# Kernel optimization log

Measured on AMD Instinct MI355X. Metric: run time of the kernel, lower is better.

Reference implementation:

```python
import jax, jax.numpy as jnp
import numpy as np

TIME_MASK_MAX_LEN = 35
TIME_MASK_STEP = 100
FREQ_MASK_MAX_LEN = 30
P = 0.5
LOG_EPS = np.float32(np.log(np.finfo(np.float64).eps))  # log(torch.finfo(float).eps)


def setup_inputs() -> dict:
    key = jax.random.key(0)
    x = jax.random.normal(key, (16, 25600, 256), dtype=jnp.float32)
    return {"x": x}


def _build_mask(key, C, T, F):
    """Boolean mask [C, T, F]; True where x is overwritten with log(eps)."""
    Cm = C - 3                      # last 3 channels are never masked
    nb = T // TIME_MASK_STEP        # number of time blocks per channel
    k1, k2, k3, k4 = jax.random.split(key, 4)
    # per (channel, block) random cutoffs, matching torch.randint semantics
    tlen = jax.random.randint(k1, (Cm, nb), 0, TIME_MASK_MAX_LEN)              # [0, 35)
    tstart = jnp.floor(jax.random.uniform(k2, (Cm, nb)) *
                       (TIME_MASK_STEP - tlen)).astype(jnp.int32)              # [0, step-len)
    flen = jax.random.randint(k3, (Cm, nb), 0, FREQ_MASK_MAX_LEN)              # [0, 30)
    fstart = jnp.floor(jax.random.uniform(k4, (Cm, nb)) *
                       (F - flen)).astype(jnp.int32)                           # [0, F-len)

    t = jnp.arange(T)
    block = t // TIME_MASK_STEP
    local = t - block * TIME_MASK_STEP                       # position within block
    valid = block < nb                                       # frames past last full block untouched
    bidx = jnp.minimum(block, nb - 1)

    ts = tstart[:, bidx]                                     # [Cm, T]
    tl = tlen[:, bidx]
    time_in = (local[None, :] >= ts) & (local[None, :] < ts + tl) & valid[None, :]

    fs = fstart[:, bidx]                                     # [Cm, T]
    fl = flen[:, bidx]
    f = jnp.arange(F)
    mask = time_in[:, :, None] & (f[None, None, :] >= fs[:, :, None]) & \
           (f[None, None, :] < (fs + fl)[:, :, None])        # [Cm, T, F]
    # last 3 channels unmasked
    return jnp.concatenate([mask, jnp.zeros((3, T, F), dtype=bool)], axis=0)


def reference(x):
    C, T, F = x.shape
    key = jax.random.key(42)
    kcoin, kmask = jax.random.split(key)
    apply_mask = jax.random.uniform(kcoin, ()) <= P          # np.random.rand() > p -> skip
    mask = _build_mask(kmask, C, T, F) & apply_mask
    return jnp.where(mask, LOG_EPS, x)
```

## Files before the change

### kernel.cpp

```cpp
#include <hip/hip_runtime.h>
#include <cstdint>
#include <cstddef>
#include <math.h>


#define C_TOT 16
#define C_MASKED 13
#define T_TOT 25600
#define F_TOT 256
#define NB 256
#define TSTEP 100

static constexpr float LOG_EPS = -36.04365338911715f;

typedef float f32x4 __attribute__((ext_vector_type(4)));

struct U2 { unsigned a, b; };

__host__ __device__ constexpr unsigned rotl_(unsigned x, int d) {
  return (x << d) | (x >> (32 - d));
}

__host__ __device__ constexpr U2 tf(unsigned k0, unsigned k1, unsigned x0, unsigned x1) {
  const unsigned ks2 = k0 ^ k1 ^ 0x1BD11BDAu;
  x0 += k0; x1 += k1;
  x0 += x1; x1 = rotl_(x1,13) ^ x0;
  x0 += x1; x1 = rotl_(x1,15) ^ x0;
  x0 += x1; x1 = rotl_(x1,26) ^ x0;
  x0 += x1; x1 = rotl_(x1, 6) ^ x0;
  x0 += k1; x1 += ks2 + 1u;
  x0 += x1; x1 = rotl_(x1,17) ^ x0;
  x0 += x1; x1 = rotl_(x1,29) ^ x0;
  x0 += x1; x1 = rotl_(x1,16) ^ x0;
  x0 += x1; x1 = rotl_(x1,24) ^ x0;
  x0 += ks2; x1 += k0 + 2u;
  x0 += x1; x1 = rotl_(x1,13) ^ x0;
  x0 += x1; x1 = rotl_(x1,15) ^ x0;
  x0 += x1; x1 = rotl_(x1,26) ^ x0;
  x0 += x1; x1 = rotl_(x1, 6) ^ x0;
  x0 += k0; x1 += k1 + 3u;
  x0 += x1; x1 = rotl_(x1,17) ^ x0;
  x0 += x1; x1 = rotl_(x1,29) ^ x0;
  x0 += x1; x1 = rotl_(x1,16) ^ x0;
  x0 += x1; x1 = rotl_(x1,24) ^ x0;
  x0 += k1; x1 += ks2 + 4u;
  x0 += x1; x1 = rotl_(x1,13) ^ x0;
  x0 += x1; x1 = rotl_(x1,15) ^ x0;
  x0 += x1; x1 = rotl_(x1,26) ^ x0;
  x0 += x1; x1 = rotl_(x1, 6) ^ x0;
  x0 += ks2; x1 += k0 + 5u;
  return U2{x0, x1};
}

constexpr U2 KCOIN = tf(0u, 42u, 0u, 0u);
constexpr U2 KMASK = tf(0u, 42u, 0u, 1u);
constexpr U2 K1 = tf(KMASK.a, KMASK.b, 0u, 0u);
constexpr U2 K2 = tf(KMASK.a, KMASK.b, 0u, 1u);
constexpr U2 K3 = tf(KMASK.a, KMASK.b, 0u, 2u);
constexpr U2 K4 = tf(KMASK.a, KMASK.b, 0u, 3u);
constexpr U2 CE = tf(KCOIN.a, KCOIN.b, 0u, 0u);
constexpr unsigned COIN_BITS = CE.a ^ CE.b;
constexpr bool APPLY = (COIN_BITS >> 9) <= 4194304u;

__device__ __forceinline__ float u01(unsigned bits) {
  return __uint_as_float((bits >> 9) | 0x3f800000u) - 1.0f;
}

__device__ __forceinline__ void mask_params(int j, int& ts, int& te, int& fs, int& fe) {
  const unsigned uj = (unsigned)j;
  unsigned h, l, bits;
  U2 e;
  e = tf(K1.a, K1.b, 0u, uj);          h = e.a ^ e.b;
  e = tf(K1.a, K1.b, 0u, uj + 3328u);  l = e.a ^ e.b;
  const unsigned tl = ((h % 35u) * 11u + (l % 35u)) % 35u;
  e = tf(K2.a, K2.b, 0u, uj);          bits = e.a ^ e.b;
  const int tstart = (int)floorf(u01(bits) * (float)(TSTEP - (int)tl));
  e = tf(K3.a, K3.b, 0u, uj);          h = e.a ^ e.b;
  e = tf(K3.a, K3.b, 0u, uj + 3328u);  l = e.a ^ e.b;
  const unsigned fl = ((h % 30u) * 16u + (l % 30u)) % 30u;
  e = tf(K4.a, K4.b, 0u, uj);          bits = e.a ^ e.b;
  const int fstart = (int)floorf(u01(bits) * (float)(F_TOT - (int)fl));
  ts = tstart; te = tstart + (int)tl;
  fs = fstart; fe = fstart + (int)fl;
}

__global__ void __launch_bounds__(256)
speca_kernel(const float* __restrict__ x, float* __restrict__ y) {
  const int bid = blockIdx.x;
  const int c = bid >> 8;
  const int b = bid & 255;
  const size_t base = ((size_t)c * T_TOT + (size_t)b * TSTEP) * F_TOT;
  const f32x4* __restrict__ in4 = (const f32x4*)(x + base);
  f32x4* __restrict__ o4 = (f32x4*)(y + base);

  int ts = 0, te = -1, fs = 0, fe = -1;
  if (APPLY && c < C_MASKED) {
    mask_params((c << 8) | b, ts, te, fs, fe);
  }

  const int tid = (int)threadIdx.x;
#pragma unroll 5
  for (int k = 0; k < (TSTEP * F_TOT) / 4 / 256; ++k) {
    const int i = k * 256 + tid;
    f32x4 v = __builtin_nontemporal_load(&in4[i]);
    const int r = i >> 6;
    if (r >= ts && r < te) {
      const int f0 = (i & 63) << 2;
      if (f0     >= fs && f0     < fe) v[0] = LOG_EPS;
      if (f0 + 1 >= fs && f0 + 1 < fe) v[1] = LOG_EPS;
      if (f0 + 2 >= fs && f0 + 2 < fe) v[2] = LOG_EPS;
      if (f0 + 3 >= fs && f0 + 3 < fe) v[3] = LOG_EPS;
    }
    __builtin_nontemporal_store(v, &o4[i]);
  }
}

extern "C" void kernel_launch(void* const* d_in, const int* in_sizes, int n_in,
                              void* d_out, int out_size, void* d_ws, size_t ws_size,
                              hipStream_t stream) {
  const float* x = (const float*)d_in[0];
  float* y = (float*)d_out;
  hipLaunchKernelGGL(speca_kernel, dim3(C_TOT * NB), dim3(256), 0, stream, x, y);
}
```

Before: 155.1 us.

## Replace fused mask kernel with device memcpy plus sparse patch kernel

The full streaming read-modify-write kernel is replaced by a hipMemcpyAsync device-to-device copy of the whole tensor, followed by a small kernel that writes LOG_EPS only into the masked rectangles. Each patch block recomputes its mask parameters and stores at most about 35x30 floats. This hands the bulk traffic to the runtime copy path (possibly a DMA engine or a tuned blit kernel) and drops the per-element mask checks, at the cost of a second launch and a dependency on how fast the copy path is.

```diff
diff --git a/kernel.cpp b/kernel.cpp
--- a/kernel.cpp
+++ b/kernel.cpp
@@ -12,8 +12,6 @@
 #define TSTEP 100
 
 static constexpr float LOG_EPS = -36.04365338911715f;
-
-typedef float f32x4 __attribute__((ext_vector_type(4)));
 
 struct U2 { unsigned a, b; };
 
@@ -84,34 +82,18 @@
   fs = fstart; fe = fstart + (int)fl;
 }
 
-__global__ void __launch_bounds__(256)
-speca_kernel(const float* __restrict__ x, float* __restrict__ y) {
+__global__ void __launch_bounds__(64)
+patch_kernel(float* __restrict__ y) {
   const int bid = blockIdx.x;
   const int c = bid >> 8;
   const int b = bid & 255;
-  const size_t base = ((size_t)c * T_TOT + (size_t)b * TSTEP) * F_TOT;
-  const f32x4* __restrict__ in4 = (const f32x4*)(x + base);
-  f32x4* __restrict__ o4 = (f32x4*)(y + base);
-
-  int ts = 0, te = -1, fs = 0, fe = -1;
-  if (APPLY && c < C_MASKED) {
-    mask_params((c << 8) | b, ts, te, fs, fe);
-  }
-
-  const int tid = (int)threadIdx.x;
-#pragma unroll 5
-  for (int k = 0; k < (TSTEP * F_TOT) / 4 / 256; ++k) {
-    const int i = k * 256 + tid;
-    f32x4 v = __builtin_nontemporal_load(&in4[i]);
-    const int r = i >> 6;
-    if (r >= ts && r < te) {
-      const int f0 = (i & 63) << 2;
-      if (f0     >= fs && f0     < fe) v[0] = LOG_EPS;
-      if (f0 + 1 >= fs && f0 + 1 < fe) v[1] = LOG_EPS;
-      if (f0 + 2 >= fs && f0 + 2 < fe) v[2] = LOG_EPS;
-      if (f0 + 3 >= fs && f0 + 3 < fe) v[3] = LOG_EPS;
-    }
-    __builtin_nontemporal_store(v, &o4[i]);
+  int ts, te, fs, fe;
+  mask_params(bid, ts, te, fs, fe);
+  const int f = fs + (int)threadIdx.x;
+  if (f >= fe) return;
+  float* __restrict__ chunk = y + ((size_t)c * T_TOT + (size_t)b * TSTEP) * F_TOT;
+  for (int r = ts; r < te; ++r) {
+    chunk[(size_t)r * F_TOT + f] = LOG_EPS;
   }
 }
 
@@ -120,5 +102,9 @@
                               hipStream_t stream) {
   const float* x = (const float*)d_in[0];
   float* y = (float*)d_out;
-  hipLaunchKernelGGL(speca_kernel, dim3(C_TOT * NB), dim3(256), 0, stream, x, y);
+  const size_t nbytes = (size_t)C_TOT * T_TOT * F_TOT * sizeof(float);
+  hipMemcpyAsync(y, x, nbytes, hipMemcpyDeviceToDevice, stream);
+  if (APPLY) {
+    hipLaunchKernelGGL(patch_kernel, dim3(C_MASKED * NB), dim3(64), 0, stream, y);
+  }
 }
```

Measured after the change: 169.8 us. 9.5% more time.
